# Performance work log

Measured on AMD Instinct MI355X. Metric: run time of the kernel, lower is better.

Reference implementation:

```python
import jax, jax.numpy as jnp
import numpy as np

N, E, T, D = 50000, 800000, 400000, 64


def _linear_params(key, fan_in, fan_out):
    kw, kb = jax.random.split(key)
    s = 1.0 / np.sqrt(fan_in)
    W = jax.random.uniform(kw, (fan_in, fan_out), minval=-s, maxval=s, dtype=jnp.float32)
    b = jax.random.uniform(kb, (fan_out,), minval=-s, maxval=s, dtype=jnp.float32)
    return W, b


def setup_inputs() -> dict:
    key = jax.random.key(0)
    ks = jax.random.split(key, 11)
    Ws1, bs1 = _linear_params(ks[0], 2 * D, D)
    Ws2, bs2 = _linear_params(ks[1], D, 3 * D)
    Wc1, bc1 = _linear_params(ks[2], 2 * D, D)
    Wc2, bc2 = _linear_params(ks[3], D, D)
    WV, bV = _linear_params(ks[4], D, D)
    return {
        "node_scalar": jax.random.normal(ks[5], (N, D), dtype=jnp.float32),
        "node_chiral": jax.random.normal(ks[6], (N, D), dtype=jnp.float32),
        "node_vector": jax.random.normal(ks[7], (N, 3, D), dtype=jnp.float32),
        "pos": jax.random.normal(ks[8], (N, 3), dtype=jnp.float32),
        "edge_index": jax.random.randint(ks[9], (E, 2), 0, N, dtype=jnp.int64),
        "triplet_index": jax.random.randint(ks[10], (T, 4), 0, N, dtype=jnp.int64),
        "Ws1": Ws1, "bs1": bs1, "Ws2": Ws2, "bs2": bs2,
        "Wc1": Wc1, "bc1": bc1, "Wc2": Wc2, "bc2": bc2,
        "WV": WV, "bV": bV,
    }


def reference(node_scalar, node_chiral, node_vector, pos, edge_index, triplet_index,
              Ws1, bs1, Ws2, bs2, Wc1, bc1, Wc2, bc2, WV, bV):
    n = node_scalar.shape[0]
    d = node_scalar.shape[1]
    e0, e1 = edge_index[:, 0], edge_index[:, 1]

    # Scalar / vector section: gather -> Linear-SiLU-Linear gate -> scatter-add
    g = jax.nn.silu(jnp.concatenate([node_scalar[e0], node_scalar[e1]], axis=1) @ Ws1 + bs1) @ Ws2 + bs2
    gate_vector, gate_edge, messages_ss = jnp.split(g, 3, axis=1)  # each [E, d]
    messages_vv = gate_vector[:, None, :] * node_vector[e1]               # [E, 3, d]
    rel = pos[e1] - pos[e0]                                               # [E, 3]
    messages_ev = gate_edge[:, None, :] * rel[:, :, None]                 # [E, 3, d]
    msg_ss = jax.ops.segment_sum(messages_ss, e0, num_segments=n)
    msg_vv = jax.ops.segment_sum(messages_vv, e0, num_segments=n)
    msg_ev = jax.ops.segment_sum(messages_ev, e0, num_segments=n)

    Vv = node_vector @ WV + bV          # [N, 3, d]
    Vv_norm = jnp.linalg.norm(Vv, axis=1)  # [N, d] (norm over spatial axis)
    message_vs = node_scalar * Vv_norm

    # Chiral section: triplet gathers, shared gate MLP, scalar triple product
    base, t1, t2, t3 = (triplet_index[:, i] for i in range(4))
    hc_base = node_chiral[base]

    def cgate(other):
        h = jnp.concatenate([hc_base, node_chiral[other]], axis=1)
        return jax.nn.silu(h @ Wc1 + bc1) @ Wc2 + bc2

    chiral_gate = cgate(t1) + cgate(t2) + cgate(t3)  # [T, d]
    pb = pos[base]
    r1, r2, r3 = pb - pos[t1], pb - pos[t2], pb - pos[t3]
    stp = jnp.einsum('ei,ei->e', r1, jnp.cross(r2, r3))  # scalar triple product [T]
    chiral_messages = chiral_gate / (stp + 0.01)[:, None]
    msg_chiral = jax.ops.segment_sum(chiral_messages, base, num_segments=n)

    return (node_scalar + msg_ss + message_vs,
            node_chiral + msg_chiral,
            node_vector + msg_vv + msg_ev)
```

## Files before the change

### kernel.cpp

```cpp
#include <hip/hip_runtime.h>
#include <math.h>

#define DD 64
typedef unsigned short ushort_t;
typedef __attribute__((ext_vector_type(8))) short bf16x8;
typedef __attribute__((ext_vector_type(4))) float f32x4;

#define GEPW 16
#define TPW 8
#define EGRID 4096
#define TGRID 2048

__device__ __forceinline__ float silu_f(float x) {
    return x / (1.0f + __expf(-x));
}

__device__ __forceinline__ unsigned f32_to_bf16_rne(float x) {
    unsigned u = __float_as_uint(x);
    unsigned r = ((u >> 16) & 1u) + 0x7fffu;
    return (u + r) >> 16;
}

__device__ __forceinline__ float bf16_to_f32(ushort_t v) {
    return __uint_as_float(((unsigned)v) << 16);
}

__device__ __forceinline__ float2 bf2_lo_hi(unsigned u) {
    return make_float2(__uint_as_float(u << 16), __uint_as_float(u & 0xffff0000u));
}

__device__ __forceinline__ void gload_lds4(const void* gsrc, void* lds_base) {
    __builtin_amdgcn_global_load_lds(
        (const __attribute__((address_space(1))) void*)gsrc,
        (__attribute__((address_space(3))) void*)lds_base,
        4, 0, 0);
}

#define RFL(x) __builtin_amdgcn_readfirstlane(x)

__global__ __launch_bounds__(256) void hist_kernel(const int* __restrict__ eidx,
                                                   int* __restrict__ counts, int E) {
    int i = blockIdx.x * 256 + threadIdx.x;
    if (i < E) atomicAdd(&counts[((const int2*)eidx)[i].x], 1);
}

__global__ __launch_bounds__(1024) void scan_kernel(const int* __restrict__ counts,
                                                    int* __restrict__ cursor, int N) {
    __shared__ int part[1024];
    int tid = threadIdx.x;
    int CH = (N + 1023) / 1024;
    int lo = tid * CH, hi = lo + CH; if (hi > N) hi = N; if (lo > N) lo = N;
    int s = 0;
    for (int i = lo; i < hi; ++i) s += counts[i];
    part[tid] = s;
    __syncthreads();
    for (int d = 1; d < 1024; d <<= 1) {
        int v = (tid >= d) ? part[tid - d] : 0;
        __syncthreads();
        part[tid] += v;
        __syncthreads();
    }
    int run = (tid == 0) ? 0 : part[tid - 1];
    for (int i = lo; i < hi; ++i) {
        cursor[i] = run;
        run += counts[i];
    }
}

__global__ __launch_bounds__(256) void fused_prep_kernel(
    const int* __restrict__ eidx, const float* __restrict__ pos,
    int* __restrict__ cursor, int2* __restrict__ eperm, float* __restrict__ relg,
    const float* __restrict__ ns, const float* __restrict__ nc,
    const float* __restrict__ Ws1, const float* __restrict__ Wc1,
    ushort_t* __restrict__ Abf, ushort_t* __restrict__ Bbf,
    float* __restrict__ C, float* __restrict__ Dm, float* __restrict__ out1,
    const float* __restrict__ nv, const float* __restrict__ WV, const float* __restrict__ bV,
    float* __restrict__ out0, float* __restrict__ out2,
    unsigned* __restrict__ nv01p, ushort_t* __restrict__ nv2bf,
    int N, int E, int sblocks)
{
    __shared__ __align__(16) char smem[69632];
    int tid = threadIdx.x;
    int bx = blockIdx.x;

    if (bx < sblocks) {
        int i = bx * 256 + tid;
        if (i < E) {
            int2 p = ((const int2*)eidx)[i];
            int dst = atomicAdd(&cursor[p.x], 1);
            eperm[dst] = p;
            relg[3 * (size_t)dst + 0] = pos[(size_t)p.y * 3 + 0] - pos[(size_t)p.x * 3 + 0];
            relg[3 * (size_t)dst + 1] = pos[(size_t)p.y * 3 + 1] - pos[(size_t)p.x * 3 + 1];
            relg[3 * (size_t)dst + 2] = pos[(size_t)p.y * 3 + 2] - pos[(size_t)p.x * 3 + 2];
        }
        return;
    }
    if (bx < sblocks + 2048) {
        int blk = bx - sblocks;
        float* w1   = (float*)smem;
        float* wc1s = (float*)(smem + 32768);
        float* xs   = (float*)(smem + 65536);
        float* ys   = (float*)(smem + 67584);
        for (int i = tid; i < 128 * 64 / 4; i += 256) {
            ((float4*)w1)[i]   = ((const float4*)Ws1)[i];
            ((float4*)wc1s)[i] = ((const float4*)Wc1)[i];
        }
        __syncthreads();
        int wave = tid >> 6, lane = tid & 63;
        for (int nb = blk * 8; nb < N; nb += 2048 * 8) {
            int n0 = nb + wave * 2;
            #pragma unroll
            for (int s = 0; s < 2; ++s) {
                int n = n0 + s;
                float xv = 0.f, yv = 0.f;
                if (n < N) { xv = ns[(size_t)n * DD + lane]; yv = nc[(size_t)n * DD + lane]; }
                xs[(wave * 2 + s) * 64 + lane] = xv;
                ys[(wave * 2 + s) * 64 + lane] = yv;
            }
            float aA[2] = {0.f, 0.f}, aB[2] = {0.f, 0.f}, aC[2] = {0.f, 0.f}, aD[2] = {0.f, 0.f};
            for (int k = 0; k < 64; ++k) {
                float wa  = w1[k * 64 + lane];
                float wb  = w1[(64 + k) * 64 + lane];
                float wca = wc1s[k * 64 + lane];
                float wcb = wc1s[(64 + k) * 64 + lane];
                #pragma unroll
                for (int s = 0; s < 2; ++s) {
                    float xk = xs[(wave * 2 + s) * 64 + k];
                    float yk = ys[(wave * 2 + s) * 64 + k];
                    aA[s] += xk * wa;  aB[s] += xk * wb;
                    aC[s] += yk * wca; aD[s] += yk * wcb;
                }
            }
            #pragma unroll
            for (int s = 0; s < 2; ++s) {
                int n = n0 + s;
                if (n < N) {
                    Abf[(size_t)n * DD + lane] = (ushort_t)f32_to_bf16_rne(aA[s]);
                    Bbf[(size_t)n * DD + lane] = (ushort_t)f32_to_bf16_rne(aB[s]);
                    C[(size_t)n * DD + lane]  = aC[s];
                    Dm[(size_t)n * DD + lane] = aD[s];
                    out1[(size_t)n * DD + lane] = ys[(wave * 2 + s) * 64 + lane];
                }
            }
            __syncthreads();
        }
        return;
    }
    {
        int blk = bx - sblocks - 2048;
        float* wv = (float*)smem;
        float* vs = (float*)(smem + 16384);
        for (int i = tid; i < 64 * 64 / 4; i += 256)
            ((float4*)wv)[i] = ((const float4*)WV)[i];
        __syncthreads();
        int wave = tid >> 6, lane = tid & 63;
        float bVj = bV[lane];
        for (int nb = blk * 8; nb < N; nb += 2048 * 8) {
            int n0 = nb + wave * 2;
            #pragma unroll
            for (int s = 0; s < 2; ++s) {
                int n = n0 + s;
                float v0 = 0.f, v1 = 0.f, v2 = 0.f;
                if (n < N) {
                    v0 = nv[((size_t)n * 3 + 0) * DD + lane];
                    v1 = nv[((size_t)n * 3 + 1) * DD + lane];
                    v2 = nv[((size_t)n * 3 + 2) * DD + lane];
                }
                vs[((wave * 2 + s) * 3 + 0) * 64 + lane] = v0;
                vs[((wave * 2 + s) * 3 + 1) * 64 + lane] = v1;
                vs[((wave * 2 + s) * 3 + 2) * 64 + lane] = v2;
            }
            float a0[2], a1[2], a2[2];
            #pragma unroll
            for (int s = 0; s < 2; ++s) { a0[s] = bVj; a1[s] = bVj; a2[s] = bVj; }
            for (int k = 0; k < 64; ++k) {
                float w = wv[k * 64 + lane];
                #pragma unroll
                for (int s = 0; s < 2; ++s) {
                    a0[s] += vs[((wave * 2 + s) * 3 + 0) * 64 + k] * w;
                    a1[s] += vs[((wave * 2 + s) * 3 + 1) * 64 + k] * w;
                    a2[s] += vs[((wave * 2 + s) * 3 + 2) * 64 + k] * w;
                }
            }
            #pragma unroll
            for (int s = 0; s < 2; ++s) {
                int n = n0 + s;
                if (n < N) {
                    float norm = sqrtf(a0[s] * a0[s] + a1[s] * a1[s] + a2[s] * a2[s]);
                    float x = ns[(size_t)n * DD + lane];
                    out0[(size_t)n * DD + lane] = x * (1.f + norm);
                    float v0 = vs[((wave * 2 + s) * 3 + 0) * 64 + lane];
                    float v1 = vs[((wave * 2 + s) * 3 + 1) * 64 + lane];
                    float v2 = vs[((wave * 2 + s) * 3 + 2) * 64 + lane];
                    out2[((size_t)n * 3 + 0) * DD + lane] = v0;
                    out2[((size_t)n * 3 + 1) * DD + lane] = v1;
                    out2[((size_t)n * 3 + 2) * DD + lane] = v2;
                    nv01p[(size_t)n * DD + lane] = f32_to_bf16_rne(v0) | (f32_to_bf16_rne(v1) << 16);
                    nv2bf[(size_t)n * DD + lane] = (ushort_t)f32_to_bf16_rne(v2);
                }
            }
            __syncthreads();
        }
    }
}

__global__ __launch_bounds__(256) void fused_et_kernel(
    const ushort_t* __restrict__ Abf, const ushort_t* __restrict__ Bbf,
    const unsigned* __restrict__ nv01p, const ushort_t* __restrict__ nv2bf,
    const float* __restrict__ relg, const int2* __restrict__ eperm,
    const float* __restrict__ bs1, const float* __restrict__ Ws2, const float* __restrict__ bs2,
    const float* __restrict__ C, const float* __restrict__ Dm,
    const float* __restrict__ pos, const int* __restrict__ tidx,
    const float* __restrict__ bc1, const float* __restrict__ Wc2, const float* __restrict__ bc2,
    float* __restrict__ out0, float* __restrict__ out1, float* __restrict__ out2,
    int E, int T)
{
    __shared__ __align__(16) char smem[50432];
    int tid = threadIdx.x;

    if (blockIdx.x < EGRID) {
        unsigned* w2frag = (unsigned*)smem;
        ushort_t* stAB   = (ushort_t*)(smem + 24576);
        ushort_t* stNV2  = (ushort_t*)(smem + 40960);
        float*    relL   = (float*)(smem + 49408);
        for (int i = tid; i < 12 * 2 * 64; i += 256) {
            int t  = i >> 7;
            int kk = (i >> 6) & 1;
            int l  = i & 63;
            int k0 = kk * 32 + (l >> 4) * 8;
            int col = t * 16 + (l & 15);
            #pragma unroll
            for (int jp = 0; jp < 4; ++jp) {
                float a = Ws2[(size_t)(k0 + 2 * jp) * 192 + col];
                float b = Ws2[(size_t)(k0 + 2 * jp + 1) * 192 + col];
                w2frag[i * 4 + jp] = f32_to_bf16_rne(a) | (f32_to_bf16_rne(b) << 16);
            }
        }
        __syncthreads();
        int wave = RFL(tid >> 6);
        int lane = tid & 63;
        float b1 = bs1[lane];
        float b2v_t[4], b2e_t[4], b2s_t[4];
        #pragma unroll
        for (int t = 0; t < 4; ++t) {
            b2v_t[t] = bs2[t * 16 + (lane & 15)];
            b2e_t[t] = bs2[64 + t * 16 + (lane & 15)];
            b2s_t[t] = bs2[128 + t * 16 + (lane & 15)];
        }
        int bid = blockIdx.x;
        int cpx = EGRID >> 3;
        int swz = (bid & 7) * cpx + (bid >> 3);

        long nG = ((long)E + GEPW - 1) / GEPW;
        for (long g = (long)swz * 4 + wave; g < nG; g += (long)EGRID * 4) {
            long e0b = g * GEPW;
            int i0a[GEPW], i1a[GEPW];
            #pragma unroll
            for (int e = 0; e < GEPW; ++e) {
                long eid = e0b + e; if (eid >= E) eid = E - 1;
                int2 p = eperm[eid];
                i0a[e] = RFL(p.x); i1a[e] = RFL(p.y);
            }
            int vi_all = 0, vi1_all = 0;
            #pragma unroll
            for (int e = 0; e < GEPW; ++e) {
                vi_all  = (lane == e) ? i0a[e] : vi_all;
                vi1_all = (lane == e) ? i1a[e] : vi1_all;
            }
            #pragma unroll
            for (int e = 0; e < GEPW; ++e) {
                const char* srcAB = (lane < 32)
                    ? ((const char*)Abf + (size_t)i0a[e] * 128 + lane * 4)
                    : ((const char*)Bbf + (size_t)i1a[e] * 128 + (lane - 32) * 4);
                gload_lds4(srcAB, stAB + (wave * GEPW + e) * 128);
            }
            __builtin_amdgcn_sched_barrier(0);
            #pragma unroll
            for (int p2 = 0; p2 < GEPW / 2; ++p2) {
                const char* src2 = (lane < 32)
                    ? ((const char*)nv2bf + (size_t)i1a[2 * p2] * 128 + lane * 4)
                    : ((const char*)nv2bf + (size_t)i1a[2 * p2 + 1] * 128 + (lane - 32) * 4);
                gload_lds4(src2, stNV2 + (wave * (GEPW / 2) + p2) * 132);
            }
            gload_lds4((const char*)relg + e0b * 12 + lane * 4, relL + wave * 64);
            int eL0 = (lane >> 4) * 4;
            unsigned nv01r[4][4];
            #pragma unroll
            for (int rg = 0; rg < 4; ++rg) {
                int i1s = __builtin_amdgcn_ds_bpermute((eL0 + rg) * 4, vi1_all);
                const char* basep = (const char*)nv01p + (size_t)(unsigned)i1s * 256 + (lane & 15) * 4;
                nv01r[rg][0] = *(const unsigned*)(basep);
                nv01r[rg][1] = *(const unsigned*)(basep + 64);
                nv01r[rg][2] = *(const unsigned*)(basep + 128);
                nv01r[rg][3] = *(const unsigned*)(basep + 192);
            }
            __builtin_amdgcn_sched_barrier(0);
            asm volatile("s_waitcnt vmcnt(25)" ::: "memory");
            __builtin_amdgcn_sched_barrier(0);
            #pragma unroll
            for (int e = 0; e < GEPW; ++e) {
                float a = bf16_to_f32(stAB[(wave * GEPW + e) * 128 + lane]);
                float b = bf16_to_f32(stAB[(wave * GEPW + e) * 128 + 64 + lane]);
                float h = silu_f(a + b + b1);
                *(float*)((char*)(stAB + (wave * GEPW + e) * 128) + ((lane * 4) ^ ((e & 7) << 5))) = h;
            }
            __builtin_amdgcn_sched_barrier(0);
            f32x4 acc[12];
            f32x4 zz = {0.f, 0.f, 0.f, 0.f};
            #pragma unroll
            for (int t = 0; t < 12; ++t) acc[t] = zz;
            int row = lane & 15;
            #pragma unroll
            for (int kk = 0; kk < 2; ++kk) {
                int coff = (kk * 128 + ((lane >> 4) * 32)) ^ ((row & 7) << 5);
                const char* hp = (const char*)(stAB + (wave * GEPW + row) * 128) + coff;
                float4 lo = *(const float4*)hp;
                float4 hi = *(const float4*)(hp + 16);
                unsigned a0, a1, a2, a3;
                asm("v_cvt_pk_bf16_f32 %0, %1, %2" : "=v"(a0) : "v"(lo.x), "v"(lo.y));
                asm("v_cvt_pk_bf16_f32 %0, %1, %2" : "=v"(a1) : "v"(lo.z), "v"(lo.w));
                asm("v_cvt_pk_bf16_f32 %0, %1, %2" : "=v"(a2) : "v"(hi.x), "v"(hi.y));
                asm("v_cvt_pk_bf16_f32 %0, %1, %2" : "=v"(a3) : "v"(hi.z), "v"(hi.w));
                union { unsigned u[4]; bf16x8 v; } af;
                af.u[0] = a0; af.u[1] = a1; af.u[2] = a2; af.u[3] = a3;
                #pragma unroll
                for (int t = 0; t < 12; ++t) {
                    bf16x8 bf = *(const bf16x8*)&w2frag[((t * 2 + kk) * 64 + lane) * 4];
                    acc[t] = __builtin_amdgcn_mfma_f32_16x16x32_bf16(af.v, bf, acc[t], 0, 0, 0);
                }
            }
            asm volatile("s_waitcnt vmcnt(0)" ::: "memory");
            __builtin_amdgcn_sched_barrier(0);
            float aS[4]  = {0.f, 0.f, 0.f, 0.f};
            float aV0[4] = {0.f, 0.f, 0.f, 0.f};
            float aV1[4] = {0.f, 0.f, 0.f, 0.f};
            float aV2[4] = {0.f, 0.f, 0.f, 0.f};
            int icur = __builtin_amdgcn_ds_bpermute(eL0 * 4, vi_all);
            #pragma unroll
            for (int rg = 0; rg < 4; ++rg) {
                int e = eL0 + rg;
                int i0 = __builtin_amdgcn_ds_bpermute(e * 4, vi_all);
                bool ok = (e0b + e) < E;
                if (i0 != icur) {
                    #pragma unroll
                    for (int t = 0; t < 4; ++t) {
                        int dim = t * 16 + (lane & 15);
                        unsafeAtomicAdd(&out0[(size_t)(unsigned)icur * 64u + dim], aS[t]);
                        unsafeAtomicAdd(&out2[((size_t)(unsigned)icur * 3u + 0) * 64u + dim], aV0[t]);
                        unsafeAtomicAdd(&out2[((size_t)(unsigned)icur * 3u + 1) * 64u + dim], aV1[t]);
                        unsafeAtomicAdd(&out2[((size_t)(unsigned)icur * 3u + 2) * 64u + dim], aV2[t]);
                        aS[t] = 0.f; aV0[t] = 0.f; aV1[t] = 0.f; aV2[t] = 0.f;
                    }
                    icur = i0;
                }
                if (ok) {
                    float r0v = relL[wave * 64 + e * 3 + 0];
                    float r1v = relL[wave * 64 + e * 3 + 1];
                    float r2v = relL[wave * 64 + e * 3 + 2];
                    #pragma unroll
                    for (int t = 0; t < 4; ++t) {
                        int dim = t * 16 + (lane & 15);
                        float gv = acc[t][rg]     + b2v_t[t];
                        float ge = acc[4 + t][rg] + b2e_t[t];
                        float ss = acc[8 + t][rg] + b2s_t[t];
                        float2 vv = bf2_lo_hi(nv01r[rg][t]);
                        float v2 = bf16_to_f32(stNV2[(wave * (GEPW / 2) + (e >> 1)) * 132 + (e & 1) * 64 + dim]);
                        aS[t]  += ss;
                        aV0[t] += gv * vv.x + ge * r0v;
                        aV1[t] += gv * vv.y + ge * r1v;
                        aV2[t] += gv * v2   + ge * r2v;
                    }
                }
            }
            #pragma unroll
            for (int t = 0; t < 4; ++t) {
                int dim = t * 16 + (lane & 15);
                unsafeAtomicAdd(&out0[(size_t)(unsigned)icur * 64u + dim], aS[t]);
                unsafeAtomicAdd(&out2[((size_t)(unsigned)icur * 3u + 0) * 64u + dim], aV0[t]);
                unsafeAtomicAdd(&out2[((size_t)(unsigned)icur * 3u + 1) * 64u + dim], aV1[t]);
                unsafeAtomicAdd(&out2[((size_t)(unsigned)icur * 3u + 2) * 64u + dim], aV2[t]);
            }
        }
        return;
    }

    {
        float* wT  = (float*)smem;
        float* stC = (float*)(smem + 16384);
        float* stD = (float*)(smem + 24576);
        for (int i = tid; i < 64 * 64 / 4; i += 256)
            ((float4*)wT)[i] = ((const float4*)Wc2)[i];
        __syncthreads();
        int wave = RFL(tid >> 6);
        int lane = tid & 63;
        float b1 = bc1[lane];
        float b2 = bc2[lane] * 3.0f;
        long tb = blockIdx.x - EGRID;
        for (long bb = tb * (4 * TPW); bb < T; bb += (long)TGRID * (4 * TPW)) {
            long t0 = bb + wave * TPW;
            int ib[TPW], it1[TPW], it2[TPW], it3[TPW];
            #pragma unroll
            for (int e = 0; e < TPW; ++e) {
                long t = t0 + e;
                int b = 0, t1 = 0, t2 = 0, t3 = 0;
                if (t < T) { int4 q = ((const int4*)tidx)[t]; b = q.x; t1 = q.y; t2 = q.z; t3 = q.w; }
                ib[e]  = RFL(b);
                it1[e] = RFL(t1);
                it2[e] = RFL(t2);
                it3[e] = RFL(t3);
            }
            #pragma unroll
            for (int e = 0; e < TPW; ++e) {
                gload_lds4(C  + (size_t)ib[e]  * DD + lane, stC + (wave * TPW + e) * 64);
                gload_lds4(Dm + (size_t)it1[e] * DD + lane, stD + ((wave * TPW + e) * 3 + 0) * 64);
                gload_lds4(Dm + (size_t)it2[e] * DD + lane, stD + ((wave * TPW + e) * 3 + 1) * 64);
                gload_lds4(Dm + (size_t)it3[e] * DD + lane, stD + ((wave * TPW + e) * 3 + 2) * 64);
            }
            asm volatile("s_waitcnt vmcnt(0)" ::: "memory");
            float inv[TPW];
            #pragma unroll
            for (int e = 0; e < TPW; ++e) {
                float hb = stC[(wave * TPW + e) * 64 + lane] + b1;
                float h = silu_f(hb + stD[((wave * TPW + e) * 3 + 0) * 64 + lane])
                        + silu_f(hb + stD[((wave * TPW + e) * 3 + 1) * 64 + lane])
                        + silu_f(hb + stD[((wave * TPW + e) * 3 + 2) * 64 + lane]);
                stC[(wave * TPW + e) * 64 + lane] = h;
                int b = ib[e], t1 = it1[e], t2 = it2[e], t3 = it3[e];
                double pbx = pos[(size_t)b * 3], pby = pos[(size_t)b * 3 + 1], pbz = pos[(size_t)b * 3 + 2];
                double r1x = pbx - pos[(size_t)t1 * 3], r1y = pby - pos[(size_t)t1 * 3 + 1], r1z = pbz - pos[(size_t)t1 * 3 + 2];
                double r2x = pbx - pos[(size_t)t2 * 3], r2y = pby - pos[(size_t)t2 * 3 + 1], r2z = pbz - pos[(size_t)t2 * 3 + 2];
                double r3x = pbx - pos[(size_t)t3 * 3], r3y = pby - pos[(size_t)t3 * 3 + 1], r3z = pbz - pos[(size_t)t3 * 3 + 2];
                double cx = r2y * r3z - r2z * r3y;
                double cy = r2z * r3x - r2x * r3z;
                double cz = r2x * r3y - r2y * r3x;
                double stp = r1x * cx + r1y * cy + r1z * cz;
                inv[e] = (float)(1.0 / (stp + 0.01));
            }
            float acc[TPW];
            #pragma unroll
            for (int e = 0; e < TPW; ++e) acc[e] = 0.f;
            for (int k4 = 0; k4 < 64; k4 += 4) {
                float4 hk[TPW];
                #pragma unroll
                for (int e = 0; e < TPW; ++e) hk[e] = *(const float4*)&stC[(wave * TPW + e) * 64 + k4];
                #pragma unroll
                for (int kk = 0; kk < 4; ++kk) {
                    float wk = wT[(k4 + kk) * 64 + lane];
                    #pragma unroll
                    for (int e = 0; e < TPW; ++e) acc[e] += (&hk[e].x)[kk] * wk;
                }
            }
            #pragma unroll
            for (int e = 0; e < TPW; ++e) {
                long t = t0 + e;
                if (t >= T) break;
                unsafeAtomicAdd(&out1[(size_t)ib[e] * DD + lane], (acc[e] + b2) * inv[e]);
            }
        }
    }
}

extern "C" void kernel_launch(void* const* d_in, const int* in_sizes, int n_in,
                              void* d_out, int out_size, void* d_ws, size_t ws_size,
                              hipStream_t stream)
{
    const float* ns  = (const float*)d_in[0];
    const float* nc  = (const float*)d_in[1];
    const float* nv  = (const float*)d_in[2];
    const float* pos = (const float*)d_in[3];
    const int* eidx  = (const int*)d_in[4];
    const int* tidx  = (const int*)d_in[5];
    const float* Ws1 = (const float*)d_in[6];
    const float* bs1 = (const float*)d_in[7];
    const float* Ws2 = (const float*)d_in[8];
    const float* bs2 = (const float*)d_in[9];
    const float* Wc1 = (const float*)d_in[10];
    const float* bc1 = (const float*)d_in[11];
    const float* Wc2 = (const float*)d_in[12];
    const float* bc2 = (const float*)d_in[13];
    const float* WV  = (const float*)d_in[14];
    const float* bV  = (const float*)d_in[15];

    int N = in_sizes[0] / 64;
    int E = in_sizes[4] / 2;
    int T = in_sizes[5] / 4;

    float* out0 = (float*)d_out;
    float* out1 = out0 + (size_t)N * 64;
    float* out2 = out1 + (size_t)N * 64;

    float* C    = (float*)d_ws;
    float* Dm   = C + (size_t)N * 64;
    float* relg = Dm + (size_t)N * 64;
    int2* eperm = (int2*)(relg + (size_t)E * 3 + 64);
    int* counts = (int*)(eperm + (size_t)E);
    int* cursor = counts + N;
    unsigned* nv01p = (unsigned*)(cursor + N);
    ushort_t* Abf   = (ushort_t*)(nv01p + (size_t)N * 64);
    ushort_t* Bbf   = Abf + (size_t)N * 64;
    ushort_t* nv2bf = Bbf + (size_t)N * 64;

    int sblocks = (E + 255) / 256;

    hipMemsetAsync(counts, 0, (size_t)N * sizeof(int), stream);
    hist_kernel<<<sblocks, 256, 0, stream>>>(eidx, counts, E);
    scan_kernel<<<1, 1024, 0, stream>>>(counts, cursor, N);
    fused_prep_kernel<<<sblocks + 4096, 256, 0, stream>>>(
        eidx, pos, cursor, eperm, relg,
        ns, nc, Ws1, Wc1, Abf, Bbf, C, Dm, out1,
        nv, WV, bV, out0, out2, nv01p, nv2bf,
        N, E, sblocks);
    fused_et_kernel<<<EGRID + TGRID, 256, 0, stream>>>(
        Abf, Bbf, nv01p, nv2bf, relg, eperm,
        bs1, Ws2, bs2,
        C, Dm, pos, tidx, bc1, Wc2, bc2,
        out0, out1, out2, E, T);
}
```

Measured before the change: 994.6 us.

## Store chiral gate projections in bf16 and split edge/triplet into separate kernels

The chiral first-layer projections C and Dm are now stored as bf16 instead of fp32. This halves the gather traffic in the triplet pass, which loads four rows per triplet. The fused edge+triplet kernel is split into two kernels launched back to back, each with its own smaller shared-memory footprint, and the triplet kernel now processes 16 triplets per wave instead of 8. Risks are extra bf16 rounding error in the chiral gate and losing the concurrency between edge and triplet work that the single fused launch provided.

```diff
diff --git a/kernel.cpp b/kernel.cpp
--- a/kernel.cpp
+++ b/kernel.cpp
@@ -7,9 +7,7 @@
 typedef __attribute__((ext_vector_type(4))) float f32x4;
 
 #define GEPW 16
-#define TPW 8
-#define EGRID 4096
-#define TGRID 2048
+#define TPW 16
 
 __device__ __forceinline__ float silu_f(float x) {
     return x / (1.0f + __expf(-x));
@@ -73,7 +71,7 @@
     const float* __restrict__ ns, const float* __restrict__ nc,
     const float* __restrict__ Ws1, const float* __restrict__ Wc1,
     ushort_t* __restrict__ Abf, ushort_t* __restrict__ Bbf,
-    float* __restrict__ C, float* __restrict__ Dm, float* __restrict__ out1,
+    ushort_t* __restrict__ Cbf, ushort_t* __restrict__ Dmbf, float* __restrict__ out1,
     const float* __restrict__ nv, const float* __restrict__ WV, const float* __restrict__ bV,
     float* __restrict__ out0, float* __restrict__ out2,
     unsigned* __restrict__ nv01p, ushort_t* __restrict__ nv2bf,
@@ -135,10 +133,10 @@
             for (int s = 0; s < 2; ++s) {
                 int n = n0 + s;
                 if (n < N) {
-                    Abf[(size_t)n * DD + lane] = (ushort_t)f32_to_bf16_rne(aA[s]);
-                    Bbf[(size_t)n * DD + lane] = (ushort_t)f32_to_bf16_rne(aB[s]);
-                    C[(size_t)n * DD + lane]  = aC[s];
-                    Dm[(size_t)n * DD + lane] = aD[s];
+                    Abf[(size_t)n * DD + lane]  = (ushort_t)f32_to_bf16_rne(aA[s]);
+                    Bbf[(size_t)n * DD + lane]  = (ushort_t)f32_to_bf16_rne(aB[s]);
+                    Cbf[(size_t)n * DD + lane]  = (ushort_t)f32_to_bf16_rne(aC[s]);
+                    Dmbf[(size_t)n * DD + lane] = (ushort_t)f32_to_bf16_rne(aD[s]);
                     out1[(size_t)n * DD + lane] = ys[(wave * 2 + s) * 64 + lane];
                 }
             }
@@ -204,258 +202,261 @@
     }
 }
 
-__global__ __launch_bounds__(256) void fused_et_kernel(
+__global__ __launch_bounds__(256) void edge_kernel(
     const ushort_t* __restrict__ Abf, const ushort_t* __restrict__ Bbf,
     const unsigned* __restrict__ nv01p, const ushort_t* __restrict__ nv2bf,
     const float* __restrict__ relg, const int2* __restrict__ eperm,
     const float* __restrict__ bs1, const float* __restrict__ Ws2, const float* __restrict__ bs2,
-    const float* __restrict__ C, const float* __restrict__ Dm,
+    float* __restrict__ out0, float* __restrict__ out2, int E)
+{
+    __shared__ __align__(16) unsigned w2frag[12 * 2 * 64 * 4];
+    __shared__ __align__(16) ushort_t stAB[4][GEPW][128];
+    __shared__ __align__(16) ushort_t stNV2[4][GEPW / 2][132];
+    __shared__ __align__(16) float    relL[4][64];
+    int tid = threadIdx.x;
+    for (int i = tid; i < 12 * 2 * 64; i += 256) {
+        int t  = i >> 7;
+        int kk = (i >> 6) & 1;
+        int l  = i & 63;
+        int k0 = kk * 32 + (l >> 4) * 8;
+        int col = t * 16 + (l & 15);
+        #pragma unroll
+        for (int jp = 0; jp < 4; ++jp) {
+            float a = Ws2[(size_t)(k0 + 2 * jp) * 192 + col];
+            float b = Ws2[(size_t)(k0 + 2 * jp + 1) * 192 + col];
+            w2frag[i * 4 + jp] = f32_to_bf16_rne(a) | (f32_to_bf16_rne(b) << 16);
+        }
+    }
+    __syncthreads();
+    int wave = RFL(tid >> 6);
+    int lane = tid & 63;
+    float b1 = bs1[lane];
+    float b2v_t[4], b2e_t[4], b2s_t[4];
+    #pragma unroll
+    for (int t = 0; t < 4; ++t) {
+        b2v_t[t] = bs2[t * 16 + (lane & 15)];
+        b2e_t[t] = bs2[64 + t * 16 + (lane & 15)];
+        b2s_t[t] = bs2[128 + t * 16 + (lane & 15)];
+    }
+
+    int bid = blockIdx.x;
+    int cpx = (int)(gridDim.x >> 3);
+    int swz = (bid & 7) * cpx + (bid >> 3);
+
+    long nG = ((long)E + GEPW - 1) / GEPW;
+    for (long g = (long)swz * 4 + wave; g < nG; g += (long)gridDim.x * 4) {
+        long e0b = g * GEPW;
+        int i0a[GEPW], i1a[GEPW];
+        #pragma unroll
+        for (int e = 0; e < GEPW; ++e) {
+            long eid = e0b + e; if (eid >= E) eid = E - 1;
+            int2 p = eperm[eid];
+            i0a[e] = RFL(p.x); i1a[e] = RFL(p.y);
+        }
+        int vi_all = 0, vi1_all = 0;
+        #pragma unroll
+        for (int e = 0; e < GEPW; ++e) {
+            vi_all  = (lane == e) ? i0a[e] : vi_all;
+            vi1_all = (lane == e) ? i1a[e] : vi1_all;
+        }
+        #pragma unroll
+        for (int e = 0; e < GEPW; ++e) {
+            const char* srcAB = (lane < 32)
+                ? ((const char*)Abf + (size_t)i0a[e] * 128 + lane * 4)
+                : ((const char*)Bbf + (size_t)i1a[e] * 128 + (lane - 32) * 4);
+            gload_lds4(srcAB, &stAB[wave][e][0]);
+        }
+        __builtin_amdgcn_sched_barrier(0);
+        #pragma unroll
+        for (int p2 = 0; p2 < GEPW / 2; ++p2) {
+            const char* src2 = (lane < 32)
+                ? ((const char*)nv2bf + (size_t)i1a[2 * p2] * 128 + lane * 4)
+                : ((const char*)nv2bf + (size_t)i1a[2 * p2 + 1] * 128 + (lane - 32) * 4);
+            gload_lds4(src2, &stNV2[wave][p2][0]);
+        }
+        gload_lds4((const char*)relg + e0b * 12 + lane * 4, &relL[wave][0]);
+        int eL0 = (lane >> 4) * 4;
+        unsigned nv01r[4][4];
+        #pragma unroll
+        for (int rg = 0; rg < 4; ++rg) {
+            int i1s = __builtin_amdgcn_ds_bpermute((eL0 + rg) * 4, vi1_all);
+            const char* basep = (const char*)nv01p + (size_t)(unsigned)i1s * 256 + (lane & 15) * 4;
+            nv01r[rg][0] = *(const unsigned*)(basep);
+            nv01r[rg][1] = *(const unsigned*)(basep + 64);
+            nv01r[rg][2] = *(const unsigned*)(basep + 128);
+            nv01r[rg][3] = *(const unsigned*)(basep + 192);
+        }
+        __builtin_amdgcn_sched_barrier(0);
+        asm volatile("s_waitcnt vmcnt(25)" ::: "memory");
+        __builtin_amdgcn_sched_barrier(0);
+        #pragma unroll
+        for (int e = 0; e < GEPW; ++e) {
+            float a = bf16_to_f32(stAB[wave][e][lane]);
+            float b = bf16_to_f32(stAB[wave][e][64 + lane]);
+            float h = silu_f(a + b + b1);
+            *(float*)((char*)&stAB[wave][e][0] + ((lane * 4) ^ ((e & 7) << 5))) = h;
+        }
+        __builtin_amdgcn_sched_barrier(0);
+        f32x4 acc[12];
+        f32x4 zz = {0.f, 0.f, 0.f, 0.f};
+        #pragma unroll
+        for (int t = 0; t < 12; ++t) acc[t] = zz;
+        int row = lane & 15;
+        #pragma unroll
+        for (int kk = 0; kk < 2; ++kk) {
+            int coff = (kk * 128 + ((lane >> 4) * 32)) ^ ((row & 7) << 5);
+            const char* hp = (const char*)&stAB[wave][row][0] + coff;
+            float4 lo = *(const float4*)hp;
+            float4 hi = *(const float4*)(hp + 16);
+            unsigned a0, a1, a2, a3;
+            asm("v_cvt_pk_bf16_f32 %0, %1, %2" : "=v"(a0) : "v"(lo.x), "v"(lo.y));
+            asm("v_cvt_pk_bf16_f32 %0, %1, %2" : "=v"(a1) : "v"(lo.z), "v"(lo.w));
+            asm("v_cvt_pk_bf16_f32 %0, %1, %2" : "=v"(a2) : "v"(hi.x), "v"(hi.y));
+            asm("v_cvt_pk_bf16_f32 %0, %1, %2" : "=v"(a3) : "v"(hi.z), "v"(hi.w));
+            union { unsigned u[4]; bf16x8 v; } af;
+            af.u[0] = a0; af.u[1] = a1; af.u[2] = a2; af.u[3] = a3;
+            #pragma unroll
+            for (int t = 0; t < 12; ++t) {
+                bf16x8 bf = *(const bf16x8*)&w2frag[((t * 2 + kk) * 64 + lane) * 4];
+                acc[t] = __builtin_amdgcn_mfma_f32_16x16x32_bf16(af.v, bf, acc[t], 0, 0, 0);
+            }
+        }
+        asm volatile("s_waitcnt vmcnt(0)" ::: "memory");
+        __builtin_amdgcn_sched_barrier(0);
+        float aS[4]  = {0.f, 0.f, 0.f, 0.f};
+        float aV0[4] = {0.f, 0.f, 0.f, 0.f};
+        float aV1[4] = {0.f, 0.f, 0.f, 0.f};
+        float aV2[4] = {0.f, 0.f, 0.f, 0.f};
+        int icur = __builtin_amdgcn_ds_bpermute(eL0 * 4, vi_all);
+        #pragma unroll
+        for (int rg = 0; rg < 4; ++rg) {
+            int e = eL0 + rg;
+            int i0 = __builtin_amdgcn_ds_bpermute(e * 4, vi_all);
+            bool ok = (e0b + e) < E;
+            if (i0 != icur) {
+                #pragma unroll
+                for (int t = 0; t < 4; ++t) {
+                    int dim = t * 16 + (lane & 15);
+                    unsafeAtomicAdd(&out0[(size_t)(unsigned)icur * 64u + dim], aS[t]);
+                    unsafeAtomicAdd(&out2[((size_t)(unsigned)icur * 3u + 0) * 64u + dim], aV0[t]);
+                    unsafeAtomicAdd(&out2[((size_t)(unsigned)icur * 3u + 1) * 64u + dim], aV1[t]);
+                    unsafeAtomicAdd(&out2[((size_t)(unsigned)icur * 3u + 2) * 64u + dim], aV2[t]);
+                    aS[t] = 0.f; aV0[t] = 0.f; aV1[t] = 0.f; aV2[t] = 0.f;
+                }
+                icur = i0;
+            }
+            if (ok) {
+                float r0v = relL[wave][e * 3 + 0];
+                float r1v = relL[wave][e * 3 + 1];
+                float r2v = relL[wave][e * 3 + 2];
+                #pragma unroll
+                for (int t = 0; t < 4; ++t) {
+                    int dim = t * 16 + (lane & 15);
+                    float gv = acc[t][rg]     + b2v_t[t];
+                    float ge = acc[4 + t][rg] + b2e_t[t];
+                    float ss = acc[8 + t][rg] + b2s_t[t];
+                    float2 vv = bf2_lo_hi(nv01r[rg][t]);
+                    float v2 = bf16_to_f32(stNV2[wave][e >> 1][(e & 1) * 64 + dim]);
+                    aS[t]  += ss;
+                    aV0[t] += gv * vv.x + ge * r0v;
+                    aV1[t] += gv * vv.y + ge * r1v;
+                    aV2[t] += gv * v2   + ge * r2v;
+                }
+            }
+        }
+        #pragma unroll
+        for (int t = 0; t < 4; ++t) {
+            int dim = t * 16 + (lane & 15);
+            unsafeAtomicAdd(&out0[(size_t)(unsigned)icur * 64u + dim], aS[t]);
+            unsafeAtomicAdd(&out2[((size_t)(unsigned)icur * 3u + 0) * 64u + dim], aV0[t]);
+            unsafeAtomicAdd(&out2[((size_t)(unsigned)icur * 3u + 1) * 64u + dim], aV1[t]);
+            unsafeAtomicAdd(&out2[((size_t)(unsigned)icur * 3u + 2) * 64u + dim], aV2[t]);
+        }
+    }
+}
+
+__global__ __launch_bounds__(256) void triplet_kernel(
+    const ushort_t* __restrict__ Cbf, const ushort_t* __restrict__ Dmbf,
     const float* __restrict__ pos, const int* __restrict__ tidx,
     const float* __restrict__ bc1, const float* __restrict__ Wc2, const float* __restrict__ bc2,
-    float* __restrict__ out0, float* __restrict__ out1, float* __restrict__ out2,
-    int E, int T)
+    float* __restrict__ out1, int T)
 {
-    __shared__ __align__(16) char smem[50432];
+    __shared__ __align__(16) float wT[64 * 64];
+    __shared__ __align__(16) ushort_t stCD[4][TPW][128];
+    __shared__ __align__(16) ushort_t stDD[4][TPW][128];
     int tid = threadIdx.x;
-
-    if (blockIdx.x < EGRID) {
-        unsigned* w2frag = (unsigned*)smem;
-        ushort_t* stAB   = (ushort_t*)(smem + 24576);
-        ushort_t* stNV2  = (ushort_t*)(smem + 40960);
-        float*    relL   = (float*)(smem + 49408);
-        for (int i = tid; i < 12 * 2 * 64; i += 256) {
-            int t  = i >> 7;
-            int kk = (i >> 6) & 1;
-            int l  = i & 63;
-            int k0 = kk * 32 + (l >> 4) * 8;
-            int col = t * 16 + (l & 15);
-            #pragma unroll
-            for (int jp = 0; jp < 4; ++jp) {
-                float a = Ws2[(size_t)(k0 + 2 * jp) * 192 + col];
-                float b = Ws2[(size_t)(k0 + 2 * jp + 1) * 192 + col];
-                w2frag[i * 4 + jp] = f32_to_bf16_rne(a) | (f32_to_bf16_rne(b) << 16);
-            }
-        }
-        __syncthreads();
-        int wave = RFL(tid >> 6);
-        int lane = tid & 63;
-        float b1 = bs1[lane];
-        float b2v_t[4], b2e_t[4], b2s_t[4];
-        #pragma unroll
-        for (int t = 0; t < 4; ++t) {
-            b2v_t[t] = bs2[t * 16 + (lane & 15)];
-            b2e_t[t] = bs2[64 + t * 16 + (lane & 15)];
-            b2s_t[t] = bs2[128 + t * 16 + (lane & 15)];
-        }
-        int bid = blockIdx.x;
-        int cpx = EGRID >> 3;
-        int swz = (bid & 7) * cpx + (bid >> 3);
-
-        long nG = ((long)E + GEPW - 1) / GEPW;
-        for (long g = (long)swz * 4 + wave; g < nG; g += (long)EGRID * 4) {
-            long e0b = g * GEPW;
-            int i0a[GEPW], i1a[GEPW];
-            #pragma unroll
-            for (int e = 0; e < GEPW; ++e) {
-                long eid = e0b + e; if (eid >= E) eid = E - 1;
-                int2 p = eperm[eid];
-                i0a[e] = RFL(p.x); i1a[e] = RFL(p.y);
-            }
-            int vi_all = 0, vi1_all = 0;
-            #pragma unroll
-            for (int e = 0; e < GEPW; ++e) {
-                vi_all  = (lane == e) ? i0a[e] : vi_all;
-                vi1_all = (lane == e) ? i1a[e] : vi1_all;
-            }
-            #pragma unroll
-            for (int e = 0; e < GEPW; ++e) {
-                const char* srcAB = (lane < 32)
-                    ? ((const char*)Abf + (size_t)i0a[e] * 128 + lane * 4)
-                    : ((const char*)Bbf + (size_t)i1a[e] * 128 + (lane - 32) * 4);
-                gload_lds4(srcAB, stAB + (wave * GEPW + e) * 128);
-            }
-            __builtin_amdgcn_sched_barrier(0);
-            #pragma unroll
-            for (int p2 = 0; p2 < GEPW / 2; ++p2) {
-                const char* src2 = (lane < 32)
-                    ? ((const char*)nv2bf + (size_t)i1a[2 * p2] * 128 + lane * 4)
-                    : ((const char*)nv2bf + (size_t)i1a[2 * p2 + 1] * 128 + (lane - 32) * 4);
-                gload_lds4(src2, stNV2 + (wave * (GEPW / 2) + p2) * 132);
-            }
-            gload_lds4((const char*)relg + e0b * 12 + lane * 4, relL + wave * 64);
-            int eL0 = (lane >> 4) * 4;
-            unsigned nv01r[4][4];
-            #pragma unroll
-            for (int rg = 0; rg < 4; ++rg) {
-                int i1s = __builtin_amdgcn_ds_bpermute((eL0 + rg) * 4, vi1_all);
-                const char* basep = (const char*)nv01p + (size_t)(unsigned)i1s * 256 + (lane & 15) * 4;
-                nv01r[rg][0] = *(const unsigned*)(basep);
-                nv01r[rg][1] = *(const unsigned*)(basep + 64);
-                nv01r[rg][2] = *(const unsigned*)(basep + 128);
-                nv01r[rg][3] = *(const unsigned*)(basep + 192);
-            }
-            __builtin_amdgcn_sched_barrier(0);
-            asm volatile("s_waitcnt vmcnt(25)" ::: "memory");
-            __builtin_amdgcn_sched_barrier(0);
-            #pragma unroll
-            for (int e = 0; e < GEPW; ++e) {
-                float a = bf16_to_f32(stAB[(wave * GEPW + e) * 128 + lane]);
-                float b = bf16_to_f32(stAB[(wave * GEPW + e) * 128 + 64 + lane]);
-                float h = silu_f(a + b + b1);
-                *(float*)((char*)(stAB + (wave * GEPW + e) * 128) + ((lane * 4) ^ ((e & 7) << 5))) = h;
-            }
-            __builtin_amdgcn_sched_barrier(0);
-            f32x4 acc[12];
-            f32x4 zz = {0.f, 0.f, 0.f, 0.f};
-            #pragma unroll
-            for (int t = 0; t < 12; ++t) acc[t] = zz;
-            int row = lane & 15;
-            #pragma unroll
-            for (int kk = 0; kk < 2; ++kk) {
-                int coff = (kk * 128 + ((lane >> 4) * 32)) ^ ((row & 7) << 5);
-                const char* hp = (const char*)(stAB + (wave * GEPW + row) * 128) + coff;
-                float4 lo = *(const float4*)hp;
-                float4 hi = *(const float4*)(hp + 16);
-                unsigned a0, a1, a2, a3;
-                asm("v_cvt_pk_bf16_f32 %0, %1, %2" : "=v"(a0) : "v"(lo.x), "v"(lo.y));
-                asm("v_cvt_pk_bf16_f32 %0, %1, %2" : "=v"(a1) : "v"(lo.z), "v"(lo.w));
-                asm("v_cvt_pk_bf16_f32 %0, %1, %2" : "=v"(a2) : "v"(hi.x), "v"(hi.y));
-                asm("v_cvt_pk_bf16_f32 %0, %1, %2" : "=v"(a3) : "v"(hi.z), "v"(hi.w));
-                union { unsigned u[4]; bf16x8 v; } af;
-                af.u[0] = a0; af.u[1] = a1; af.u[2] = a2; af.u[3] = a3;
-                #pragma unroll
-                for (int t = 0; t < 12; ++t) {
-                    bf16x8 bf = *(const bf16x8*)&w2frag[((t * 2 + kk) * 64 + lane) * 4];
-                    acc[t] = __builtin_amdgcn_mfma_f32_16x16x32_bf16(af.v, bf, acc[t], 0, 0, 0);
-                }
-            }
-            asm volatile("s_waitcnt vmcnt(0)" ::: "memory");
-            __builtin_amdgcn_sched_barrier(0);
-            float aS[4]  = {0.f, 0.f, 0.f, 0.f};
-            float aV0[4] = {0.f, 0.f, 0.f, 0.f};
-            float aV1[4] = {0.f, 0.f, 0.f, 0.f};
-            float aV2[4] = {0.f, 0.f, 0.f, 0.f};
-            int icur = __builtin_amdgcn_ds_bpermute(eL0 * 4, vi_all);
-            #pragma unroll
-            for (int rg = 0; rg < 4; ++rg) {
-                int e = eL0 + rg;
-                int i0 = __builtin_amdgcn_ds_bpermute(e * 4, vi_all);
-                bool ok = (e0b + e) < E;
-                if (i0 != icur) {
-                    #pragma unroll
-                    for (int t = 0; t < 4; ++t) {
-                        int dim = t * 16 + (lane & 15);
-                        unsafeAtomicAdd(&out0[(size_t)(unsigned)icur * 64u + dim], aS[t]);
-                        unsafeAtomicAdd(&out2[((size_t)(unsigned)icur * 3u + 0) * 64u + dim], aV0[t]);
-                        unsafeAtomicAdd(&out2[((size_t)(unsigned)icur * 3u + 1) * 64u + dim], aV1[t]);
-                        unsafeAtomicAdd(&out2[((size_t)(unsigned)icur * 3u + 2) * 64u + dim], aV2[t]);
-                        aS[t] = 0.f; aV0[t] = 0.f; aV1[t] = 0.f; aV2[t] = 0.f;
-                    }
-                    icur = i0;
-                }
-                if (ok) {
-                    float r0v = relL[wave * 64 + e * 3 + 0];
-                    float r1v = relL[wave * 64 + e * 3 + 1];
-                    float r2v = relL[wave * 64 + e * 3 + 2];
-                    #pragma unroll
-                    for (int t = 0; t < 4; ++t) {
-                        int dim = t * 16 + (lane & 15);
-                        float gv = acc[t][rg]     + b2v_t[t];
-                        float ge = acc[4 + t][rg] + b2e_t[t];
-                        float ss = acc[8 + t][rg] + b2s_t[t];
-                        float2 vv = bf2_lo_hi(nv01r[rg][t]);
-                        float v2 = bf16_to_f32(stNV2[(wave * (GEPW / 2) + (e >> 1)) * 132 + (e & 1) * 64 + dim]);
-                        aS[t]  += ss;
-                        aV0[t] += gv * vv.x + ge * r0v;
-                        aV1[t] += gv * vv.y + ge * r1v;
-                        aV2[t] += gv * v2   + ge * r2v;
-                    }
-                }
-            }
-            #pragma unroll
-            for (int t = 0; t < 4; ++t) {
-                int dim = t * 16 + (lane & 15);
-                unsafeAtomicAdd(&out0[(size_t)(unsigned)icur * 64u + dim], aS[t]);
-                unsafeAtomicAdd(&out2[((size_t)(unsigned)icur * 3u + 0) * 64u + dim], aV0[t]);
-                unsafeAtomicAdd(&out2[((size_t)(unsigned)icur * 3u + 1) * 64u + dim], aV1[t]);
-                unsafeAtomicAdd(&out2[((size_t)(unsigned)icur * 3u + 2) * 64u + dim], aV2[t]);
-            }
-        }
-        return;
-    }
-
-    {
-        float* wT  = (float*)smem;
-        float* stC = (float*)(smem + 16384);
-        float* stD = (float*)(smem + 24576);
-        for (int i = tid; i < 64 * 64 / 4; i += 256)
-            ((float4*)wT)[i] = ((const float4*)Wc2)[i];
-        __syncthreads();
-        int wave = RFL(tid >> 6);
-        int lane = tid & 63;
-        float b1 = bc1[lane];
-        float b2 = bc2[lane] * 3.0f;
-        long tb = blockIdx.x - EGRID;
-        for (long bb = tb * (4 * TPW); bb < T; bb += (long)TGRID * (4 * TPW)) {
-            long t0 = bb + wave * TPW;
-            int ib[TPW], it1[TPW], it2[TPW], it3[TPW];
+    for (int i = tid; i < 64 * 64 / 4; i += 256)
+        ((float4*)wT)[i] = ((const float4*)Wc2)[i];
+    __syncthreads();
+    int wave = RFL(tid >> 6);
+    int lane = tid & 63;
+    float b1 = bc1[lane];
+    float b2 = bc2[lane] * 3.0f;
+    for (long bb = (long)blockIdx.x * (4 * TPW); bb < T; bb += (long)gridDim.x * (4 * TPW)) {
+        long t0 = bb + wave * TPW;
+        int ib[TPW], it1[TPW], it2[TPW], it3[TPW];
+        #pragma unroll
+        for (int e = 0; e < TPW; ++e) {
+            long t = t0 + e;
+            int b = 0, t1 = 0, t2 = 0, t3 = 0;
+            if (t < T) { int4 q = ((const int4*)tidx)[t]; b = q.x; t1 = q.y; t2 = q.z; t3 = q.w; }
+            ib[e]  = RFL(b);
+            it1[e] = RFL(t1);
+            it2[e] = RFL(t2);
+            it3[e] = RFL(t3);
+        }
+        #pragma unroll
+        for (int e = 0; e < TPW; ++e) {
+            const char* srcA = (lane < 32)
+                ? ((const char*)Cbf  + (size_t)ib[e]  * 128 + lane * 4)
+                : ((const char*)Dmbf + (size_t)it1[e] * 128 + (lane - 32) * 4);
+            gload_lds4(srcA, &stCD[wave][e][0]);
+            const char* srcB = (lane < 32)
+                ? ((const char*)Dmbf + (size_t)it2[e] * 128 + lane * 4)
+                : ((const char*)Dmbf + (size_t)it3[e] * 128 + (lane - 32) * 4);
+            gload_lds4(srcB, &stDD[wave][e][0]);
+        }
+        asm volatile("s_waitcnt vmcnt(0)" ::: "memory");
+        float inv[TPW];
+        #pragma unroll
+        for (int e = 0; e < TPW; ++e) {
+            float c  = bf16_to_f32(stCD[wave][e][lane]);
+            float d1 = bf16_to_f32(stCD[wave][e][64 + lane]);
+            float d2 = bf16_to_f32(stDD[wave][e][lane]);
+            float d3 = bf16_to_f32(stDD[wave][e][64 + lane]);
+            float hb = c + b1;
+            float h = silu_f(hb + d1) + silu_f(hb + d2) + silu_f(hb + d3);
+            ((float*)&stCD[wave][e][0])[lane] = h;
+            int b = ib[e], t1 = it1[e], t2 = it2[e], t3 = it3[e];
+            double pbx = pos[(size_t)b * 3], pby = pos[(size_t)b * 3 + 1], pbz = pos[(size_t)b * 3 + 2];
+            double r1x = pbx - pos[(size_t)t1 * 3], r1y = pby - pos[(size_t)t1 * 3 + 1], r1z = pbz - pos[(size_t)t1 * 3 + 2];
+            double r2x = pbx - pos[(size_t)t2 * 3], r2y = pby - pos[(size_t)t2 * 3 + 1], r2z = pbz - pos[(size_t)t2 * 3 + 2];
+            double r3x = pbx - pos[(size_t)t3 * 3], r3y = pby - pos[(size_t)t3 * 3 + 1], r3z = pbz - pos[(size_t)t3 * 3 + 2];
+            double cx = r2y * r3z - r2z * r3y;
+            double cy = r2z * r3x - r2x * r3z;
+            double cz = r2x * r3y - r2y * r3x;
+            double stp = r1x * cx + r1y * cy + r1z * cz;
+            inv[e] = (float)(1.0 / (stp + 0.01));
+        }
+        float acc[TPW];
+        #pragma unroll
+        for (int e = 0; e < TPW; ++e) acc[e] = 0.f;
+        for (int k4 = 0; k4 < 64; k4 += 4) {
+            float w0 = wT[(k4 + 0) * 64 + lane];
+            float w1 = wT[(k4 + 1) * 64 + lane];
+            float w2 = wT[(k4 + 2) * 64 + lane];
+            float w3 = wT[(k4 + 3) * 64 + lane];
             #pragma unroll
             for (int e = 0; e < TPW; ++e) {
-                long t = t0 + e;
-                int b = 0, t1 = 0, t2 = 0, t3 = 0;
-                if (t < T) { int4 q = ((const int4*)tidx)[t]; b = q.x; t1 = q.y; t2 = q.z; t3 = q.w; }
-                ib[e]  = RFL(b);
-                it1[e] = RFL(t1);
-                it2[e] = RFL(t2);
-                it3[e] = RFL(t3);
-            }
-            #pragma unroll
-            for (int e = 0; e < TPW; ++e) {
-                gload_lds4(C  + (size_t)ib[e]  * DD + lane, stC + (wave * TPW + e) * 64);
-                gload_lds4(Dm + (size_t)it1[e] * DD + lane, stD + ((wave * TPW + e) * 3 + 0) * 64);
-                gload_lds4(Dm + (size_t)it2[e] * DD + lane, stD + ((wave * TPW + e) * 3 + 1) * 64);
-                gload_lds4(Dm + (size_t)it3[e] * DD + lane, stD + ((wave * TPW + e) * 3 + 2) * 64);
-            }
-            asm volatile("s_waitcnt vmcnt(0)" ::: "memory");
-            float inv[TPW];
-            #pragma unroll
-            for (int e = 0; e < TPW; ++e) {
-                float hb = stC[(wave * TPW + e) * 64 + lane] + b1;
-                float h = silu_f(hb + stD[((wave * TPW + e) * 3 + 0) * 64 + lane])
-                        + silu_f(hb + stD[((wave * TPW + e) * 3 + 1) * 64 + lane])
-                        + silu_f(hb + stD[((wave * TPW + e) * 3 + 2) * 64 + lane]);
-                stC[(wave * TPW + e) * 64 + lane] = h;
-                int b = ib[e], t1 = it1[e], t2 = it2[e], t3 = it3[e];
-                double pbx = pos[(size_t)b * 3], pby = pos[(size_t)b * 3 + 1], pbz = pos[(size_t)b * 3 + 2];
-                double r1x = pbx - pos[(size_t)t1 * 3], r1y = pby - pos[(size_t)t1 * 3 + 1], r1z = pbz - pos[(size_t)t1 * 3 + 2];
-                double r2x = pbx - pos[(size_t)t2 * 3], r2y = pby - pos[(size_t)t2 * 3 + 1], r2z = pbz - pos[(size_t)t2 * 3 + 2];
-                double r3x = pbx - pos[(size_t)t3 * 3], r3y = pby - pos[(size_t)t3 * 3 + 1], r3z = pbz - pos[(size_t)t3 * 3 + 2];
-                double cx = r2y * r3z - r2z * r3y;
-                double cy = r2z * r3x - r2x * r3z;
-                double cz = r2x * r3y - r2y * r3x;
-                double stp = r1x * cx + r1y * cy + r1z * cz;
-                inv[e] = (float)(1.0 / (stp + 0.01));
-            }
-            float acc[TPW];
-            #pragma unroll
-            for (int e = 0; e < TPW; ++e) acc[e] = 0.f;
-            for (int k4 = 0; k4 < 64; k4 += 4) {
-                float4 hk[TPW];
-                #pragma unroll
-                for (int e = 0; e < TPW; ++e) hk[e] = *(const float4*)&stC[(wave * TPW + e) * 64 + k4];
-                #pragma unroll
-                for (int kk = 0; kk < 4; ++kk) {
-                    float wk = wT[(k4 + kk) * 64 + lane];
-                    #pragma unroll
-                    for (int e = 0; e < TPW; ++e) acc[e] += (&hk[e].x)[kk] * wk;
-                }
-            }
-            #pragma unroll
-            for (int e = 0; e < TPW; ++e) {
-                long t = t0 + e;
-                if (t >= T) break;
-                unsafeAtomicAdd(&out1[(size_t)ib[e] * DD + lane], (acc[e] + b2) * inv[e]);
-            }
+                float4 hk = *(const float4*)&((const float*)&stCD[wave][e][0])[k4];
+                acc[e] += hk.x * w0 + hk.y * w1 + hk.z * w2 + hk.w * w3;
+            }
+        }
+        #pragma unroll
+        for (int e = 0; e < TPW; ++e) {
+            long t = t0 + e;
+            if (t >= T) break;
+            unsafeAtomicAdd(&out1[(size_t)ib[e] * DD + lane], (acc[e] + b2) * inv[e]);
         }
     }
 }
@@ -489,9 +490,7 @@
     float* out1 = out0 + (size_t)N * 64;
     float* out2 = out1 + (size_t)N * 64;
 
-    float* C    = (float*)d_ws;
-    float* Dm   = C + (size_t)N * 64;
-    float* relg = Dm + (size_t)N * 64;
+    float* relg = (float*)d_ws;
     int2* eperm = (int2*)(relg + (size_t)E * 3 + 64);
     int* counts = (int*)(eperm + (size_t)E);
     int* cursor = counts + N;
@@ -499,6 +498,8 @@
     ushort_t* Abf   = (ushort_t*)(nv01p + (size_t)N * 64);
     ushort_t* Bbf   = Abf + (size_t)N * 64;
     ushort_t* nv2bf = Bbf + (size_t)N * 64;
+    ushort_t* Cbf   = nv2bf + (size_t)N * 64;
+    ushort_t* Dmbf  = Cbf + (size_t)N * 64;
 
     int sblocks = (E + 255) / 256;
 
@@ -507,12 +508,10 @@
     scan_kernel<<<1, 1024, 0, stream>>>(counts, cursor, N);
     fused_prep_kernel<<<sblocks + 4096, 256, 0, stream>>>(
         eidx, pos, cursor, eperm, relg,
-        ns, nc, Ws1, Wc1, Abf, Bbf, C, Dm, out1,
+        ns, nc, Ws1, Wc1, Abf, Bbf, Cbf, Dmbf, out1,
         nv, WV, bV, out0, out2, nv01p, nv2bf,
         N, E, sblocks);
-    fused_et_kernel<<<EGRID + TGRID, 256, 0, stream>>>(
-        Abf, Bbf, nv01p, nv2bf, relg, eperm,
-        bs1, Ws2, bs2,
-        C, Dm, pos, tidx, bc1, Wc2, bc2,
-        out0, out1, out2, E, T);
-}
+    edge_kernel<<<4096, 256, 0, stream>>>(Abf, Bbf, nv01p, nv2bf, relg, eperm,
+                                          bs1, Ws2, bs2, out0, out2, E);
+    triplet_kernel<<<2048, 256, 0, stream>>>(Cbf, Dmbf, pos, tidx, bc1, Wc2, bc2, out1, T);
+}
```

After: 1.106 ms. 1.11x slower.
